# Optimization experiments

Hardware: AMD Instinct MI355X
Metric: run time of the kernel (lower is better)

## Reference

```python
import jax, jax.numpy as jnp
import numpy as np

N_WIRES = 4
N_LAYERS = 3
B = 65536
EPS = 1e-5


def setup_inputs() -> dict:
    key = jax.random.key(0)
    ks = jax.random.split(key, 8)
    return {
        "x": jax.random.normal(ks[0], (B, 1, 28, 28), jnp.float32),
        "pre_fc_w": jax.random.normal(ks[1], (N_WIRES, 16), jnp.float32) * 0.25,
        "pre_fc_b": jax.random.normal(ks[2], (N_WIRES,), jnp.float32) * 0.25,
        "weights": jax.random.normal(ks[3], (N_LAYERS, N_WIRES, 2), jnp.float32),
        "fc_w": jax.random.normal(ks[4], (4, N_WIRES), jnp.float32) * 0.5,
        "fc_b": jax.random.normal(ks[5], (4,), jnp.float32) * 0.5,
        "bn_gamma": jnp.ones((4,), jnp.float32),
        "bn_beta": jnp.zeros((4,), jnp.float32),
    }


def _rx_mat(theta):
    # RX(t) = [[cos t/2, -i sin t/2], [-i sin t/2, cos t/2]]; theta scalar or [B]
    half = theta * 0.5
    c = jnp.cos(half).astype(jnp.complex64)
    s = (-1j) * jnp.sin(half).astype(jnp.complex64)
    return jnp.stack([jnp.stack([c, s], -1), jnp.stack([s, c], -1)], -2)


def _rz_mat(theta):
    # RZ(t) = diag(e^{-it/2}, e^{it/2})
    half = theta * 0.5
    e = jnp.exp((-1j) * half.astype(jnp.complex64))
    z = jnp.zeros_like(e)
    return jnp.stack([jnp.stack([e, z], -1), jnp.stack([z, jnp.conj(e)], -1)], -2)


def _apply_1q(state, mat, wire):
    # state: [B,2,2,2,2]; mat: [2,2] or [B,2,2]
    s = jnp.moveaxis(state, wire + 1, -1)
    if mat.ndim == 3:
        s = jnp.einsum('bij,b...j->b...i', mat, s)
    else:
        s = jnp.einsum('ij,b...j->b...i', mat, s)
    return jnp.moveaxis(s, -1, wire + 1)


def _cnot(state, c, t):
    s = jnp.moveaxis(state, (c + 1, t + 1), (-2, -1))
    s = jnp.stack([s[..., 0, :], s[..., 1, ::-1]], axis=-2)
    return jnp.moveaxis(s, (-2, -1), (c + 1, t + 1))


def _circuit(encoded, weights):
    # encoded: [B, n_wires] angles; returns per-wire <Z> expvals [B, n_wires]
    b = encoded.shape[0]
    state = jnp.zeros((b,) + (2,) * N_WIRES, jnp.complex64).at[:, 0, 0, 0, 0].set(1.0)
    for w in range(N_WIRES):
        state = _apply_1q(state, _rx_mat(encoded[:, w]), w)
    for l in range(N_LAYERS):
        for w in range(N_WIRES):
            state = _apply_1q(state, _rx_mat(weights[l, w, 0]), w)
            state = _apply_1q(state, _rz_mat(weights[l, w, 1]), w)
        for w in range(N_WIRES):
            state = _cnot(state, w, (w + 1) % N_WIRES)
    probs = jnp.abs(state) ** 2  # [B,2,2,2,2] float32
    zvals = []
    for w in range(N_WIRES):
        shape = [1] + [2 if i == w else 1 for i in range(N_WIRES)]
        sign = jnp.array([1.0, -1.0], jnp.float32).reshape(shape)
        zvals.append(jnp.sum(probs * sign, axis=tuple(range(1, N_WIRES + 1))))
    return jnp.stack(zvals, -1)


def reference(x, pre_fc_w, pre_fc_b, weights, fc_w, fc_b, bn_gamma, bn_beta):
    bsz = x.shape[0]
    # avg_pool2d kernel=6 stride=6 (valid): windows cover the first 24x24 pixels -> 4x4
    pooled = x[:, :, :24, :24].reshape(bsz, 1, 4, 6, 4, 6).mean(axis=(3, 5)).reshape(bsz, 16)
    encoded = pooled @ pre_fc_w.T + pre_fc_b          # [B, n_wires]
    q_out = _circuit(encoded, weights)                # [B, n_wires]
    logits = q_out @ fc_w.T + fc_b                    # [B, 4]
    mean = logits.mean(axis=0)
    var = logits.var(axis=0)                          # biased var (training-mode BN)
    return (logits - mean) / jnp.sqrt(var + EPS) * bn_gamma + bn_beta
```

## Files before the change

kernel.cpp:

```cpp
#include <hip/hip_runtime.h>
#include <math.h>

#define NB 65536
#define NBLK1 2048
#define IMGS1 32

__global__ __launch_bounds__(256) void fused_kernel(
        const float* __restrict__ x,
        const float* __restrict__ pre_w,
        const float* __restrict__ pre_b,
        const float* __restrict__ weights,
        const float* __restrict__ fc_w,
        const float* __restrict__ fc_b,
        float4* __restrict__ out,
        float* __restrict__ partial) {
    __shared__ float2 Wl[256];
    __shared__ float4 enc[IMGS1];
    const int tid = threadIdx.x;

    if (tid >= 192 && tid < 208) {
        const int t = tid - 192;
        float cr[16], ci[16];
#pragma unroll
        for (int i = 0; i < 16; ++i) { cr[i] = (i == t) ? 1.0f : 0.0f; ci[i] = 0.0f; }

        for (int l = 0; l < 3; ++l) {
#pragma unroll
            for (int w = 0; w < 4; ++w) {
                const int mask = 8 >> w;
                float tx = weights[(l * 4 + w) * 2 + 0] * 0.5f;
                float c = cosf(tx), s = sinf(tx);
#pragma unroll
                for (int i = 0; i < 16; ++i) {
                    if (!(i & mask)) {
                        const int ip = i | mask;
                        float a0r = cr[i], a0i = ci[i], a1r = cr[ip], a1i = ci[ip];
                        cr[i]  = c * a0r + s * a1i;
                        ci[i]  = c * a0i - s * a1r;
                        cr[ip] = c * a1r + s * a0i;
                        ci[ip] = c * a1i - s * a0r;
                    }
                }
                float tz = weights[(l * 4 + w) * 2 + 1] * 0.5f;
                float ce = cosf(tz), se = sinf(tz);
#pragma unroll
                for (int i = 0; i < 16; ++i) {
                    if (!(i & mask)) {
                        const int ip = i | mask;
                        float a0r = cr[i], a0i = ci[i], a1r = cr[ip], a1i = ci[ip];
                        cr[i]  = ce * a0r + se * a0i;
                        ci[i]  = ce * a0i - se * a0r;
                        cr[ip] = ce * a1r - se * a1i;
                        ci[ip] = ce * a1i + se * a1r;
                    }
                }
            }
#pragma unroll
            for (int w = 0; w < 4; ++w) {
                const int mc = 8 >> w;
                const int mt = 8 >> ((w + 1) & 3);
#pragma unroll
                for (int i = 0; i < 16; ++i) {
                    if ((i & mc) && !(i & mt)) {
                        const int ip = i | mt;
                        float tr = cr[i], ti = ci[i];
                        cr[i] = cr[ip]; ci[i] = ci[ip];
                        cr[ip] = tr;   ci[ip] = ti;
                    }
                }
            }
        }
        int p = __popc(t) & 3;
#pragma unroll
        for (int i = 0; i < 16; ++i) {
            float wr, wi;
            if (p == 0)      { wr =  cr[i]; wi =  ci[i]; }
            else if (p == 1) { wr =  ci[i]; wi = -cr[i]; }
            else if (p == 2) { wr = -cr[i]; wi = -ci[i]; }
            else             { wr = -ci[i]; wi =  cr[i]; }
            Wl[i * 16 + t] = make_float2(wr, wi);
        }
    }

    const int t8 = tid & 7;
    const size_t img_idx = (size_t)blockIdx.x * IMGS1 + (tid >> 3);
    const float* img = x + img_idx * 784 + (size_t)(t8 * 3) * 28;

    float cs0 = 0.f, cs1 = 0.f, cs2 = 0.f, cs3 = 0.f;
#pragma unroll
    for (int r = 0; r < 3; ++r) {
        const float4* row = (const float4*)(img + r * 28);
        float4 f0 = row[0], f1 = row[1], f2 = row[2];
        float4 f3 = row[3], f4 = row[4], f5 = row[5];
        cs0 += f0.x + f0.y + f0.z + f0.w + f1.x + f1.y;
        cs1 += f1.z + f1.w + f2.x + f2.y + f2.z + f2.w;
        cs2 += f3.x + f3.y + f3.z + f3.w + f4.x + f4.y;
        cs3 += f4.z + f4.w + f5.x + f5.y + f5.z + f5.w;
    }
    const float inv36 = 1.0f / 36.0f;
    cs0 *= inv36; cs1 *= inv36; cs2 *= inv36; cs3 *= inv36;

    const int k0 = (t8 >> 1) * 4;
    float p0 = cs0 * pre_w[k0]      + cs1 * pre_w[k0 + 1] +
               cs2 * pre_w[k0 + 2]  + cs3 * pre_w[k0 + 3];
    float p1 = cs0 * pre_w[16 + k0] + cs1 * pre_w[16 + k0 + 1] +
               cs2 * pre_w[16 + k0 + 2] + cs3 * pre_w[16 + k0 + 3];
    float p2 = cs0 * pre_w[32 + k0] + cs1 * pre_w[32 + k0 + 1] +
               cs2 * pre_w[32 + k0 + 2] + cs3 * pre_w[32 + k0 + 3];
    float p3 = cs0 * pre_w[48 + k0] + cs1 * pre_w[48 + k0 + 1] +
               cs2 * pre_w[48 + k0 + 2] + cs3 * pre_w[48 + k0 + 3];

    p0 += __shfl_xor(p0, 1); p0 += __shfl_xor(p0, 2); p0 += __shfl_xor(p0, 4);
    p1 += __shfl_xor(p1, 1); p1 += __shfl_xor(p1, 2); p1 += __shfl_xor(p1, 4);
    p2 += __shfl_xor(p2, 1); p2 += __shfl_xor(p2, 2); p2 += __shfl_xor(p2, 4);
    p3 += __shfl_xor(p3, 1); p3 += __shfl_xor(p3, 2); p3 += __shfl_xor(p3, 4);

    if (t8 == 0) {
        enc[tid >> 3] = make_float4(p0 + pre_b[0], p1 + pre_b[1],
                                    p2 + pre_b[2], p3 + pre_b[3]);
    }
    __syncthreads();

    if (tid < IMGS1) {
        float4 e = enc[tid];
        float s0, c0, s1, c1, s2, c2, s3, c3;
        __sincosf(e.x * 0.5f, &s0, &c0);
        __sincosf(e.y * 0.5f, &s1, &c1);
        __sincosf(e.z * 0.5f, &s2, &c2);
        __sincosf(e.w * 0.5f, &s3, &c3);

        float m01[4] = { c0 * c1, c0 * s1, s0 * c1, s0 * s1 };
        float m23[4] = { c2 * c3, c2 * s3, s2 * c3, s2 * s3 };
        float m[16];
#pragma unroll
        for (int i = 0; i < 16; ++i) m[i] = m01[i >> 2] * m23[i & 3];

        float z0 = 0.f, z1 = 0.f, z2 = 0.f, z3 = 0.f;
#pragma unroll
        for (int i = 0; i < 16; ++i) {
            float sr = 0.f, si = 0.f;
#pragma unroll
            for (int j = 0; j < 16; ++j) {
                float2 w = Wl[i * 16 + j];
                sr += w.x * m[j];
                si += w.y * m[j];
            }
            float pr = sr * sr + si * si;
            z0 += (i & 8) ? -pr : pr;
            z1 += (i & 4) ? -pr : pr;
            z2 += (i & 2) ? -pr : pr;
            z3 += (i & 1) ? -pr : pr;
        }

        float l0 = fc_b[0] + fc_w[0]  * z0 + fc_w[1]  * z1 + fc_w[2]  * z2 + fc_w[3]  * z3;
        float l1 = fc_b[1] + fc_w[4]  * z0 + fc_w[5]  * z1 + fc_w[6]  * z2 + fc_w[7]  * z3;
        float l2 = fc_b[2] + fc_w[8]  * z0 + fc_w[9]  * z1 + fc_w[10] * z2 + fc_w[11] * z3;
        float l3 = fc_b[3] + fc_w[12] * z0 + fc_w[13] * z1 + fc_w[14] * z2 + fc_w[15] * z3;
        out[(size_t)blockIdx.x * IMGS1 + tid] = make_float4(l0, l1, l2, l3);

        float s[8] = { l0, l1, l2, l3, l0 * l0, l1 * l1, l2 * l2, l3 * l3 };
#pragma unroll
        for (int off = 16; off; off >>= 1) {
#pragma unroll
            for (int q = 0; q < 8; ++q) s[q] += __shfl_down(s[q], off);
        }
        if (tid == 0) {
            float4* p = (float4*)(partial + (size_t)blockIdx.x * 8);
            p[0] = make_float4(s[0], s[1], s[2], s[3]);
            p[1] = make_float4(s[4], s[5], s[6], s[7]);
        }
    }
}

__global__ __launch_bounds__(256) void finalize_kernel(
        float4* __restrict__ out,
        const float* __restrict__ partial,
        const float* __restrict__ gamma,
        const float* __restrict__ beta) {
    __shared__ float red4[4][8];
    __shared__ float scsh[8];
    const int tid = threadIdx.x;

    float s[8];
#pragma unroll
    for (int q = 0; q < 8; ++q) s[q] = 0.f;
#pragma unroll
    for (int r = 0; r < NBLK1 / 256; ++r) {
        const float4* row = (const float4*)(partial + (size_t)(tid + r * 256) * 8);
        float4 a = row[0], c = row[1];
        s[0] += a.x; s[1] += a.y; s[2] += a.z; s[3] += a.w;
        s[4] += c.x; s[5] += c.y; s[6] += c.z; s[7] += c.w;
    }
#pragma unroll
    for (int off = 32; off; off >>= 1) {
#pragma unroll
        for (int q = 0; q < 8; ++q) s[q] += __shfl_down(s[q], off);
    }
    if ((tid & 63) == 0) {
#pragma unroll
        for (int q = 0; q < 8; ++q) red4[tid >> 6][q] = s[q];
    }
    __syncthreads();
    if (tid < 8) {
        red4[0][tid] = red4[0][tid] + red4[1][tid] + red4[2][tid] + red4[3][tid];
    }
    __syncthreads();
    if (tid < 4) {
        const float invB = 1.0f / (float)NB;
        float mean = red4[0][tid] * invB;
        float var  = red4[0][4 + tid] * invB - mean * mean;
        float inv  = rsqrtf(var + 1e-5f);
        float g = gamma[tid];
        scsh[tid]     = g * inv;
        scsh[4 + tid] = beta[tid] - mean * g * inv;
    }
    __syncthreads();

    const float sc0 = scsh[0], sc1 = scsh[1], sc2 = scsh[2], sc3 = scsh[3];
    const float sh0 = scsh[4], sh1 = scsh[5], sh2 = scsh[6], sh3 = scsh[7];
    const int b = blockIdx.x * 256 + tid;
    float4 v = out[b];
    v.x = v.x * sc0 + sh0;
    v.y = v.y * sc1 + sh1;
    v.z = v.z * sc2 + sh2;
    v.w = v.w * sc3 + sh3;
    out[b] = v;
}

extern "C" void kernel_launch(void* const* d_in, const int* in_sizes, int n_in,
                              void* d_out, int out_size, void* d_ws, size_t ws_size,
                              hipStream_t stream) {
    const float* x       = (const float*)d_in[0];
    const float* pre_w   = (const float*)d_in[1];
    const float* pre_b   = (const float*)d_in[2];
    const float* weights = (const float*)d_in[3];
    const float* fc_w    = (const float*)d_in[4];
    const float* fc_b    = (const float*)d_in[5];
    const float* gamma   = (const float*)d_in[6];
    const float* beta    = (const float*)d_in[7];

    float* partial = (float*)d_ws;

    hipLaunchKernelGGL(fused_kernel, dim3(NBLK1), dim3(256), 0, stream,
                       x, pre_w, pre_b, weights, fc_w, fc_b,
                       (float4*)d_out, partial);
    hipLaunchKernelGGL(finalize_kernel, dim3(NB / 256), dim3(256), 0, stream,
                       (float4*)d_out, partial, gamma, beta);
}
```

Baseline: 41.50 us.

## Fuse main and finalize kernels into one cooperative persistent kernel with grid sync

Replaces the two-kernel pipeline with a single cooperative launch. A persistent grid sized from occupancy (times 256 CUs) loops over tiles, accumulates the BN statistics per block, grid-syncs, then reduces the partials and normalises its own tiles in place. This removes the second kernel launch and its gap, and the W matrix is built once per block instead of once per tile. In exchange it pays for a grid-wide barrier and re-reads the output for normalisation. The old two-kernel path remains as a fallback.

```diff
diff --git a/kernel.cpp b/kernel.cpp
--- a/kernel.cpp
+++ b/kernel.cpp
@@ -1,91 +1,80 @@
 #include <hip/hip_runtime.h>
+#include <hip/hip_cooperative_groups.h>
 #include <math.h>
 
+namespace cg = cooperative_groups;
+
 #define NB 65536
-#define NBLK1 2048
+#define NTILES 2048
 #define IMGS1 32
 
-__global__ __launch_bounds__(256) void fused_kernel(
-        const float* __restrict__ x,
-        const float* __restrict__ pre_w,
-        const float* __restrict__ pre_b,
-        const float* __restrict__ weights,
-        const float* __restrict__ fc_w,
-        const float* __restrict__ fc_b,
-        float4* __restrict__ out,
-        float* __restrict__ partial) {
-    __shared__ float2 Wl[256];
-    __shared__ float4 enc[IMGS1];
-    const int tid = threadIdx.x;
-
-    if (tid >= 192 && tid < 208) {
-        const int t = tid - 192;
-        float cr[16], ci[16];
-#pragma unroll
-        for (int i = 0; i < 16; ++i) { cr[i] = (i == t) ? 1.0f : 0.0f; ci[i] = 0.0f; }
-
-        for (int l = 0; l < 3; ++l) {
-#pragma unroll
-            for (int w = 0; w < 4; ++w) {
-                const int mask = 8 >> w;
-                float tx = weights[(l * 4 + w) * 2 + 0] * 0.5f;
-                float c = cosf(tx), s = sinf(tx);
-#pragma unroll
-                for (int i = 0; i < 16; ++i) {
-                    if (!(i & mask)) {
-                        const int ip = i | mask;
-                        float a0r = cr[i], a0i = ci[i], a1r = cr[ip], a1i = ci[ip];
-                        cr[i]  = c * a0r + s * a1i;
-                        ci[i]  = c * a0i - s * a1r;
-                        cr[ip] = c * a1r + s * a0i;
-                        ci[ip] = c * a1i - s * a0r;
-                    }
+__device__ __forceinline__ void build_W_lane(int t, const float* __restrict__ weights,
+                                             float2* __restrict__ Wl) {
+    float cr[16], ci[16];
+#pragma unroll
+    for (int i = 0; i < 16; ++i) { cr[i] = (i == t) ? 1.0f : 0.0f; ci[i] = 0.0f; }
+
+    for (int l = 0; l < 3; ++l) {
+#pragma unroll
+        for (int w = 0; w < 4; ++w) {
+            const int mask = 8 >> w;
+            float tx = weights[(l * 4 + w) * 2 + 0] * 0.5f;
+            float c = cosf(tx), s = sinf(tx);
+#pragma unroll
+            for (int i = 0; i < 16; ++i) {
+                if (!(i & mask)) {
+                    const int ip = i | mask;
+                    float a0r = cr[i], a0i = ci[i], a1r = cr[ip], a1i = ci[ip];
+                    cr[i]  = c * a0r + s * a1i;
+                    ci[i]  = c * a0i - s * a1r;
+                    cr[ip] = c * a1r + s * a0i;
+                    ci[ip] = c * a1i - s * a0r;
                 }
-                float tz = weights[(l * 4 + w) * 2 + 1] * 0.5f;
-                float ce = cosf(tz), se = sinf(tz);
-#pragma unroll
-                for (int i = 0; i < 16; ++i) {
-                    if (!(i & mask)) {
-                        const int ip = i | mask;
-                        float a0r = cr[i], a0i = ci[i], a1r = cr[ip], a1i = ci[ip];
-                        cr[i]  = ce * a0r + se * a0i;
-                        ci[i]  = ce * a0i - se * a0r;
-                        cr[ip] = ce * a1r - se * a1i;
-                        ci[ip] = ce * a1i + se * a1r;
-                    }
+            }
+            float tz = weights[(l * 4 + w) * 2 + 1] * 0.5f;
+            float ce = cosf(tz), se = sinf(tz);
+#pragma unroll
+            for (int i = 0; i < 16; ++i) {
+                if (!(i & mask)) {
+                    const int ip = i | mask;
+                    float a0r = cr[i], a0i = ci[i], a1r = cr[ip], a1i = ci[ip];
+                    cr[i]  = ce * a0r + se * a0i;
+                    ci[i]  = ce * a0i - se * a0r;
+                    cr[ip] = ce * a1r - se * a1i;
+                    ci[ip] = ce * a1i + se * a1r;
                 }
             }
-#pragma unroll
-            for (int w = 0; w < 4; ++w) {
-                const int mc = 8 >> w;
-                const int mt = 8 >> ((w + 1) & 3);
-#pragma unroll
-                for (int i = 0; i < 16; ++i) {
-                    if ((i & mc) && !(i & mt)) {
-                        const int ip = i | mt;
-                        float tr = cr[i], ti = ci[i];
-                        cr[i] = cr[ip]; ci[i] = ci[ip];
-                        cr[ip] = tr;   ci[ip] = ti;
-                    }
+        }
+#pragma unroll
+        for (int w = 0; w < 4; ++w) {
+            const int mc = 8 >> w;
+            const int mt = 8 >> ((w + 1) & 3);
+#pragma unroll
+            for (int i = 0; i < 16; ++i) {
+                if ((i & mc) && !(i & mt)) {
+                    const int ip = i | mt;
+                    float tr = cr[i], ti = ci[i];
+                    cr[i] = cr[ip]; ci[i] = ci[ip];
+                    cr[ip] = tr;   ci[ip] = ti;
                 }
             }
         }
-        int p = __popc(t) & 3;
-#pragma unroll
-        for (int i = 0; i < 16; ++i) {
-            float wr, wi;
-            if (p == 0)      { wr =  cr[i]; wi =  ci[i]; }
-            else if (p == 1) { wr =  ci[i]; wi = -cr[i]; }
-            else if (p == 2) { wr = -cr[i]; wi = -ci[i]; }
-            else             { wr = -ci[i]; wi =  cr[i]; }
-            Wl[i * 16 + t] = make_float2(wr, wi);
-        }
-    }
-
-    const int t8 = tid & 7;
-    const size_t img_idx = (size_t)blockIdx.x * IMGS1 + (tid >> 3);
-    const float* img = x + img_idx * 784 + (size_t)(t8 * 3) * 28;
-
+    }
+    int p = __popc(t) & 3;
+#pragma unroll
+    for (int i = 0; i < 16; ++i) {
+        float wr, wi;
+        if (p == 0)      { wr =  cr[i]; wi =  ci[i]; }
+        else if (p == 1) { wr =  ci[i]; wi = -cr[i]; }
+        else if (p == 2) { wr = -cr[i]; wi = -ci[i]; }
+        else             { wr = -ci[i]; wi =  cr[i]; }
+        Wl[i * 16 + t] = make_float2(wr, wi);
+    }
+}
+
+__device__ __forceinline__ float4 pool_prefc(const float* __restrict__ img,
+                                             const float* __restrict__ pre_w,
+                                             int t8) {
     float cs0 = 0.f, cs1 = 0.f, cs2 = 0.f, cs3 = 0.f;
 #pragma unroll
     for (int r = 0; r < 3; ++r) {
@@ -101,91 +90,227 @@
     cs0 *= inv36; cs1 *= inv36; cs2 *= inv36; cs3 *= inv36;
 
     const int k0 = (t8 >> 1) * 4;
-    float p0 = cs0 * pre_w[k0]      + cs1 * pre_w[k0 + 1] +
-               cs2 * pre_w[k0 + 2]  + cs3 * pre_w[k0 + 3];
-    float p1 = cs0 * pre_w[16 + k0] + cs1 * pre_w[16 + k0 + 1] +
-               cs2 * pre_w[16 + k0 + 2] + cs3 * pre_w[16 + k0 + 3];
-    float p2 = cs0 * pre_w[32 + k0] + cs1 * pre_w[32 + k0 + 1] +
-               cs2 * pre_w[32 + k0 + 2] + cs3 * pre_w[32 + k0 + 3];
-    float p3 = cs0 * pre_w[48 + k0] + cs1 * pre_w[48 + k0 + 1] +
-               cs2 * pre_w[48 + k0 + 2] + cs3 * pre_w[48 + k0 + 3];
-
-    p0 += __shfl_xor(p0, 1); p0 += __shfl_xor(p0, 2); p0 += __shfl_xor(p0, 4);
-    p1 += __shfl_xor(p1, 1); p1 += __shfl_xor(p1, 2); p1 += __shfl_xor(p1, 4);
-    p2 += __shfl_xor(p2, 1); p2 += __shfl_xor(p2, 2); p2 += __shfl_xor(p2, 4);
-    p3 += __shfl_xor(p3, 1); p3 += __shfl_xor(p3, 2); p3 += __shfl_xor(p3, 4);
-
-    if (t8 == 0) {
-        enc[tid >> 3] = make_float4(p0 + pre_b[0], p1 + pre_b[1],
-                                    p2 + pre_b[2], p3 + pre_b[3]);
-    }
-    __syncthreads();
-
-    if (tid < IMGS1) {
-        float4 e = enc[tid];
-        float s0, c0, s1, c1, s2, c2, s3, c3;
-        __sincosf(e.x * 0.5f, &s0, &c0);
-        __sincosf(e.y * 0.5f, &s1, &c1);
-        __sincosf(e.z * 0.5f, &s2, &c2);
-        __sincosf(e.w * 0.5f, &s3, &c3);
-
-        float m01[4] = { c0 * c1, c0 * s1, s0 * c1, s0 * s1 };
-        float m23[4] = { c2 * c3, c2 * s3, s2 * c3, s2 * s3 };
-        float m[16];
-#pragma unroll
-        for (int i = 0; i < 16; ++i) m[i] = m01[i >> 2] * m23[i & 3];
-
-        float z0 = 0.f, z1 = 0.f, z2 = 0.f, z3 = 0.f;
-#pragma unroll
-        for (int i = 0; i < 16; ++i) {
-            float sr = 0.f, si = 0.f;
-#pragma unroll
-            for (int j = 0; j < 16; ++j) {
-                float2 w = Wl[i * 16 + j];
-                sr += w.x * m[j];
-                si += w.y * m[j];
-            }
-            float pr = sr * sr + si * si;
-            z0 += (i & 8) ? -pr : pr;
-            z1 += (i & 4) ? -pr : pr;
-            z2 += (i & 2) ? -pr : pr;
-            z3 += (i & 1) ? -pr : pr;
-        }
-
-        float l0 = fc_b[0] + fc_w[0]  * z0 + fc_w[1]  * z1 + fc_w[2]  * z2 + fc_w[3]  * z3;
-        float l1 = fc_b[1] + fc_w[4]  * z0 + fc_w[5]  * z1 + fc_w[6]  * z2 + fc_w[7]  * z3;
-        float l2 = fc_b[2] + fc_w[8]  * z0 + fc_w[9]  * z1 + fc_w[10] * z2 + fc_w[11] * z3;
-        float l3 = fc_b[3] + fc_w[12] * z0 + fc_w[13] * z1 + fc_w[14] * z2 + fc_w[15] * z3;
-        out[(size_t)blockIdx.x * IMGS1 + tid] = make_float4(l0, l1, l2, l3);
-
-        float s[8] = { l0, l1, l2, l3, l0 * l0, l1 * l1, l2 * l2, l3 * l3 };
-#pragma unroll
-        for (int off = 16; off; off >>= 1) {
-#pragma unroll
-            for (int q = 0; q < 8; ++q) s[q] += __shfl_down(s[q], off);
-        }
-        if (tid == 0) {
-            float4* p = (float4*)(partial + (size_t)blockIdx.x * 8);
-            p[0] = make_float4(s[0], s[1], s[2], s[3]);
-            p[1] = make_float4(s[4], s[5], s[6], s[7]);
-        }
-    }
-}
-
-__global__ __launch_bounds__(256) void finalize_kernel(
+    float4 p;
+    p.x = cs0 * pre_w[k0]      + cs1 * pre_w[k0 + 1] +
+          cs2 * pre_w[k0 + 2]  + cs3 * pre_w[k0 + 3];
+    p.y = cs0 * pre_w[16 + k0] + cs1 * pre_w[16 + k0 + 1] +
+          cs2 * pre_w[16 + k0 + 2] + cs3 * pre_w[16 + k0 + 3];
+    p.z = cs0 * pre_w[32 + k0] + cs1 * pre_w[32 + k0 + 1] +
+          cs2 * pre_w[32 + k0 + 2] + cs3 * pre_w[32 + k0 + 3];
+    p.w = cs0 * pre_w[48 + k0] + cs1 * pre_w[48 + k0 + 1] +
+          cs2 * pre_w[48 + k0 + 2] + cs3 * pre_w[48 + k0 + 3];
+    return p;
+}
+
+__device__ __forceinline__ float4 quantum_logits(float4 e,
+                                                 const float2* __restrict__ Wl,
+                                                 const float* __restrict__ fc_w,
+                                                 const float* __restrict__ fc_b) {
+    float s0, c0, s1, c1, s2, c2, s3, c3;
+    __sincosf(e.x * 0.5f, &s0, &c0);
+    __sincosf(e.y * 0.5f, &s1, &c1);
+    __sincosf(e.z * 0.5f, &s2, &c2);
+    __sincosf(e.w * 0.5f, &s3, &c3);
+
+    float m01[4] = { c0 * c1, c0 * s1, s0 * c1, s0 * s1 };
+    float m23[4] = { c2 * c3, c2 * s3, s2 * c3, s2 * s3 };
+    float m[16];
+#pragma unroll
+    for (int i = 0; i < 16; ++i) m[i] = m01[i >> 2] * m23[i & 3];
+
+    float z0 = 0.f, z1 = 0.f, z2 = 0.f, z3 = 0.f;
+#pragma unroll
+    for (int i = 0; i < 16; ++i) {
+        float sr = 0.f, si = 0.f;
+#pragma unroll
+        for (int j = 0; j < 16; ++j) {
+            float2 w = Wl[i * 16 + j];
+            sr += w.x * m[j];
+            si += w.y * m[j];
+        }
+        float pr = sr * sr + si * si;
+        z0 += (i & 8) ? -pr : pr;
+        z1 += (i & 4) ? -pr : pr;
+        z2 += (i & 2) ? -pr : pr;
+        z3 += (i & 1) ? -pr : pr;
+    }
+    float4 l;
+    l.x = fc_b[0] + fc_w[0]  * z0 + fc_w[1]  * z1 + fc_w[2]  * z2 + fc_w[3]  * z3;
+    l.y = fc_b[1] + fc_w[4]  * z0 + fc_w[5]  * z1 + fc_w[6]  * z2 + fc_w[7]  * z3;
+    l.z = fc_b[2] + fc_w[8]  * z0 + fc_w[9]  * z1 + fc_w[10] * z2 + fc_w[11] * z3;
+    l.w = fc_b[3] + fc_w[12] * z0 + fc_w[13] * z1 + fc_w[14] * z2 + fc_w[15] * z3;
+    return l;
+}
+
+__global__ __launch_bounds__(256) void fused_all(
+        const float* __restrict__ x,
+        const float* __restrict__ pre_w,
+        const float* __restrict__ pre_b,
+        const float* __restrict__ weights,
+        const float* __restrict__ fc_w,
+        const float* __restrict__ fc_b,
+        const float* __restrict__ gamma,
+        const float* __restrict__ beta,
         float4* __restrict__ out,
-        const float* __restrict__ partial,
-        const float* __restrict__ gamma,
-        const float* __restrict__ beta) {
+        float* __restrict__ partial,
+        int ntiles) {
+    __shared__ float2 Wl[256];
+    __shared__ float4 enc[2][IMGS1];
     __shared__ float red4[4][8];
     __shared__ float scsh[8];
     const int tid = threadIdx.x;
 
+    if (tid >= 192 && tid < 208) build_W_lane(tid - 192, weights, Wl);
+
+    const int t8 = tid & 7;
+    const int imgInTile = tid >> 3;
+    float a0 = 0.f, a1 = 0.f, a2 = 0.f, a3 = 0.f;
+    float a4 = 0.f, a5 = 0.f, a6 = 0.f, a7 = 0.f;
+
+    int k = 0;
+    for (int tile = blockIdx.x; tile < ntiles; tile += gridDim.x, ++k) {
+        const size_t img_idx = (size_t)tile * IMGS1 + imgInTile;
+        float4 p = pool_prefc(x + img_idx * 784 + (size_t)(t8 * 3) * 28,
+                              pre_w, t8);
+        p.x += __shfl_xor(p.x, 1); p.x += __shfl_xor(p.x, 2); p.x += __shfl_xor(p.x, 4);
+        p.y += __shfl_xor(p.y, 1); p.y += __shfl_xor(p.y, 2); p.y += __shfl_xor(p.y, 4);
+        p.z += __shfl_xor(p.z, 1); p.z += __shfl_xor(p.z, 2); p.z += __shfl_xor(p.z, 4);
+        p.w += __shfl_xor(p.w, 1); p.w += __shfl_xor(p.w, 2); p.w += __shfl_xor(p.w, 4);
+        if (t8 == 0) {
+            enc[k & 1][imgInTile] = make_float4(p.x + pre_b[0], p.y + pre_b[1],
+                                                p.z + pre_b[2], p.w + pre_b[3]);
+        }
+        __syncthreads();
+
+        if (tid < IMGS1) {
+            float4 l = quantum_logits(enc[k & 1][tid], Wl, fc_w, fc_b);
+            out[(size_t)tile * IMGS1 + tid] = l;
+
+            float s[8] = { l.x, l.y, l.z, l.w,
+                           l.x * l.x, l.y * l.y, l.z * l.z, l.w * l.w };
+#pragma unroll
+            for (int off = 16; off; off >>= 1) {
+#pragma unroll
+                for (int q = 0; q < 8; ++q) s[q] += __shfl_down(s[q], off);
+            }
+            if (tid == 0) {
+                a0 += s[0]; a1 += s[1]; a2 += s[2]; a3 += s[3];
+                a4 += s[4]; a5 += s[5]; a6 += s[6]; a7 += s[7];
+            }
+        }
+    }
+
+    if (tid == 0) {
+        float4* p = (float4*)(partial + (size_t)blockIdx.x * 8);
+        p[0] = make_float4(a0, a1, a2, a3);
+        p[1] = make_float4(a4, a5, a6, a7);
+    }
+
+    cg::this_grid().sync();
+
     float s[8];
 #pragma unroll
     for (int q = 0; q < 8; ++q) s[q] = 0.f;
-#pragma unroll
-    for (int r = 0; r < NBLK1 / 256; ++r) {
+    for (int r = tid; r < (int)gridDim.x; r += 256) {
+        const float4* row = (const float4*)(partial + (size_t)r * 8);
+        float4 a = row[0], c = row[1];
+        s[0] += a.x; s[1] += a.y; s[2] += a.z; s[3] += a.w;
+        s[4] += c.x; s[5] += c.y; s[6] += c.z; s[7] += c.w;
+    }
+#pragma unroll
+    for (int off = 32; off; off >>= 1) {
+#pragma unroll
+        for (int q = 0; q < 8; ++q) s[q] += __shfl_down(s[q], off);
+    }
+    if ((tid & 63) == 0) {
+#pragma unroll
+        for (int q = 0; q < 8; ++q) red4[tid >> 6][q] = s[q];
+    }
+    __syncthreads();
+    if (tid < 8) {
+        red4[0][tid] = red4[0][tid] + red4[1][tid] + red4[2][tid] + red4[3][tid];
+    }
+    __syncthreads();
+    if (tid < 4) {
+        const float invB = 1.0f / (float)NB;
+        float mean = red4[0][tid] * invB;
+        float var  = red4[0][4 + tid] * invB - mean * mean;
+        float inv  = rsqrtf(var + 1e-5f);
+        float g = gamma[tid];
+        scsh[tid]     = g * inv;
+        scsh[4 + tid] = beta[tid] - mean * g * inv;
+    }
+    __syncthreads();
+
+    const float sc0 = scsh[0], sc1 = scsh[1], sc2 = scsh[2], sc3 = scsh[3];
+    const float sh0 = scsh[4], sh1 = scsh[5], sh2 = scsh[6], sh3 = scsh[7];
+
+    for (int tile = blockIdx.x; tile < ntiles; tile += gridDim.x) {
+        if (tid < IMGS1) {
+            float4 v = out[(size_t)tile * IMGS1 + tid];
+            v.x = v.x * sc0 + sh0;
+            v.y = v.y * sc1 + sh1;
+            v.z = v.z * sc2 + sh2;
+            v.w = v.w * sc3 + sh3;
+            out[(size_t)tile * IMGS1 + tid] = v;
+        }
+    }
+}
+
+__global__ __launch_bounds__(256) void fused_kernel(
+        const float* __restrict__ x, const float* __restrict__ pre_w,
+        const float* __restrict__ pre_b, const float* __restrict__ weights,
+        const float* __restrict__ fc_w, const float* __restrict__ fc_b,
+        float4* __restrict__ out, float* __restrict__ partial) {
+    __shared__ float2 Wl[256];
+    __shared__ float4 enc[IMGS1];
+    const int tid = threadIdx.x;
+
+    if (tid >= 192 && tid < 208) build_W_lane(tid - 192, weights, Wl);
+
+    const int t8 = tid & 7;
+    const size_t img_idx = (size_t)blockIdx.x * IMGS1 + (tid >> 3);
+    float4 p = pool_prefc(x + img_idx * 784 + (size_t)(t8 * 3) * 28, pre_w, t8);
+    p.x += __shfl_xor(p.x, 1); p.x += __shfl_xor(p.x, 2); p.x += __shfl_xor(p.x, 4);
+    p.y += __shfl_xor(p.y, 1); p.y += __shfl_xor(p.y, 2); p.y += __shfl_xor(p.y, 4);
+    p.z += __shfl_xor(p.z, 1); p.z += __shfl_xor(p.z, 2); p.z += __shfl_xor(p.z, 4);
+    p.w += __shfl_xor(p.w, 1); p.w += __shfl_xor(p.w, 2); p.w += __shfl_xor(p.w, 4);
+    if (t8 == 0) {
+        enc[tid >> 3] = make_float4(p.x + pre_b[0], p.y + pre_b[1],
+                                    p.z + pre_b[2], p.w + pre_b[3]);
+    }
+    __syncthreads();
+
+    if (tid < IMGS1) {
+        float4 l = quantum_logits(enc[tid], Wl, fc_w, fc_b);
+        out[(size_t)blockIdx.x * IMGS1 + tid] = l;
+        float s[8] = { l.x, l.y, l.z, l.w,
+                       l.x * l.x, l.y * l.y, l.z * l.z, l.w * l.w };
+#pragma unroll
+        for (int off = 16; off; off >>= 1) {
+#pragma unroll
+            for (int q = 0; q < 8; ++q) s[q] += __shfl_down(s[q], off);
+        }
+        if (tid == 0) {
+            float4* pp = (float4*)(partial + (size_t)blockIdx.x * 8);
+            pp[0] = make_float4(s[0], s[1], s[2], s[3]);
+            pp[1] = make_float4(s[4], s[5], s[6], s[7]);
+        }
+    }
+}
+
+__global__ __launch_bounds__(256) void finalize_kernel(
+        float4* __restrict__ out, const float* __restrict__ partial,
+        const float* __restrict__ gamma, const float* __restrict__ beta) {
+    __shared__ float red4[4][8];
+    __shared__ float scsh[8];
+    const int tid = threadIdx.x;
+
+    float s[8];
+#pragma unroll
+    for (int q = 0; q < 8; ++q) s[q] = 0.f;
+#pragma unroll
+    for (int r = 0; r < NTILES / 256; ++r) {
         const float4* row = (const float4*)(partial + (size_t)(tid + r * 256) * 8);
         float4 a = row[0], c = row[1];
         s[0] += a.x; s[1] += a.y; s[2] += a.z; s[3] += a.w;
@@ -239,11 +364,29 @@
     const float* gamma   = (const float*)d_in[6];
     const float* beta    = (const float*)d_in[7];
 
+    float4* out4   = (float4*)d_out;
     float* partial = (float*)d_ws;
 
-    hipLaunchKernelGGL(fused_kernel, dim3(NBLK1), dim3(256), 0, stream,
-                       x, pre_w, pre_b, weights, fc_w, fc_b,
-                       (float4*)d_out, partial);
+    int occ = 0;
+    hipError_t qe = hipOccupancyMaxActiveBlocksPerMultiprocessor(
+        &occ, (const void*)fused_all, 256, 0);
+    if (qe == hipSuccess && occ > 0) {
+        int nblk = occ * 256;
+        if (nblk > NTILES) nblk = NTILES;
+        int ntiles = NTILES;
+        void* args[] = {
+            (void*)&x, (void*)&pre_w, (void*)&pre_b, (void*)&weights,
+            (void*)&fc_w, (void*)&fc_b, (void*)&gamma, (void*)&beta,
+            (void*)&out4, (void*)&partial, (void*)&ntiles
+        };
+        if (hipLaunchCooperativeKernel((const void*)fused_all, dim3(nblk),
+                                       dim3(256), args, 0, stream) == hipSuccess) {
+            return;
+        }
+    }
+
+    hipLaunchKernelGGL(fused_kernel, dim3(NTILES), dim3(256), 0, stream,
+                       x, pre_w, pre_b, weights, fc_w, fc_b, out4, partial);
     hipLaunchKernelGGL(finalize_kernel, dim3(NB / 256), dim3(256), 0, stream,
-                       (float4*)d_out, partial, gamma, beta);
-}
+                       out4, partial, gamma, beta);
+}
```

After: 99.84 us. +140.6%, slower.
